# Performance work log

Measured on AMD Instinct MI355X. Metric: run time of the kernel, lower is better.

## Reference

```python
import jax, jax.numpy as jnp
import numpy as np
import math

B, L, IN_DIM, OUT_DIM = 2, 2048, 128, 128
H, DH = 8, 32            # num_heads, dim_head
ED = H * DH * 2          # embed_dim = 512
DEPTH = 1
LAMBDA_INIT = 0.8 - 0.6 * math.exp(-0.3 * (DEPTH + 1))
EPS = 1e-8


def setup_inputs() -> dict:
    key = jax.random.key(0)
    ks = jax.random.split(key, 10)
    x = jax.random.normal(ks[0], (B, 1, L, IN_DIM), dtype=jnp.float32)
    mask_2d = jax.random.bernoulli(ks[1], 0.9, (B, L, L))
    Wq = jax.random.normal(ks[2], (IN_DIM, ED), dtype=jnp.float32) * 0.05
    Wkv = jax.random.normal(ks[3], (IN_DIM, 2 * ED), dtype=jnp.float32) * 0.05
    Wout = jax.random.normal(ks[4], (ED, OUT_DIM), dtype=jnp.float32) * 0.05
    lambda_q1 = jax.random.normal(ks[5], (DH,), dtype=jnp.float32) * 0.1
    lambda_k1 = jax.random.normal(ks[6], (DH,), dtype=jnp.float32) * 0.1
    lambda_q2 = jax.random.normal(ks[7], (DH,), dtype=jnp.float32) * 0.1
    lambda_k2 = jax.random.normal(ks[8], (DH,), dtype=jnp.float32) * 0.1
    gamma = jnp.ones((2 * DH,), dtype=jnp.float32)
    return {"x": x, "mask_2d": mask_2d, "Wq": Wq, "Wkv": Wkv, "Wout": Wout,
            "lambda_q1": lambda_q1, "lambda_k1": lambda_k1,
            "lambda_q2": lambda_q2, "lambda_k2": lambda_k2, "gamma": gamma}


def reference(x, mask_2d, Wq, Wkv, Wout, lambda_q1, lambda_k1, lambda_q2, lambda_k2, gamma):
    b = x.shape[0]
    xs = x[:, 0]                                   # [b, L, in_dim]
    q = xs @ Wq                                    # [b, L, 2*H*DH]
    k, v = jnp.split(xs @ Wkv, 2, axis=-1)
    q = q.reshape(b, L, 2 * H, DH).transpose(0, 2, 1, 3) * (DH ** -0.5)  # [b,2H,L,d]
    k = k.reshape(b, L, 2 * H, DH).transpose(0, 2, 1, 3)                 # [b,2H,L,d]
    v = v.reshape(b, L, H, 2 * DH).transpose(0, 2, 1, 3)                 # [b,H,L,2d]
    dots = jnp.einsum('bnld,bnmd->bnlm', q, k)     # [b,2H,L,L]
    mask_value = -jnp.finfo(dots.dtype).max
    dots = jnp.where(mask_2d[:, None, :, :], dots, mask_value)
    attn_w = jax.nn.softmax(dots.astype(jnp.float32), axis=-1).astype(dots.dtype)
    lam1 = jnp.exp(jnp.sum(lambda_q1 * lambda_k1))
    lam2 = jnp.exp(jnp.sum(lambda_q2 * lambda_k2))
    lam = lam1 - lam2 + LAMBDA_INIT
    attn_w = attn_w.reshape(b, H, 2, L, L)
    attn_w = attn_w[:, :, 0] - lam * attn_w[:, :, 1]   # [b,H,L,L]
    attn = jnp.einsum('bhlm,bhmd->bhld', attn_w, v)    # [b,H,L,2d]
    rms = jnp.sqrt(jnp.mean(attn ** 2, axis=-1, keepdims=True))
    attn = gamma * (attn / (rms + EPS)) * (1.0 - LAMBDA_INIT)
    out = attn.transpose(0, 2, 1, 3).reshape(b, L, H * 2 * DH) @ Wout  # [b,L,out_dim]
    return out[:, None]                             # [b,1,L,out_dim]
```

## Files before the change

kernel.cpp:

```cpp
#include <hip/hip_runtime.h>
#include <float.h>
#include <math.h>

typedef __attribute__((ext_vector_type(8))) short short8;
typedef __attribute__((ext_vector_type(4))) float f32x4;

constexpr int SEQL = 2048;
constexpr int NQH  = 16;
constexpr int NVH  = 8;
constexpr int DHD  = 32;
constexpr float LAMB_INIT = 0.4707130183436648f;
constexpr float REPS      = 1e-8f;
constexpr float QW        = 0.25503492f;

static __device__ __forceinline__ unsigned short f2bf(float f) {
    union { float f; unsigned u; } a; a.f = f;
    unsigned u = a.u;
    u += 0x7fffu + ((u >> 16) & 1u);
    return (unsigned short)(u >> 16);
}

static __device__ __forceinline__ unsigned cvtpk(float lo, float hi) {
    unsigned r;
    asm("v_cvt_pk_bf16_f32 %0, %1, %2" : "=v"(r) : "v"(lo), "v"(hi));
    return r;
}

static __device__ __forceinline__ float expv(float x) {
    float r;
    asm("v_exp_f32 %0, %1" : "=v"(r) : "v"(x));
    return r;
}

static __device__ __forceinline__ void stage16(const unsigned short* g, unsigned short* l) {
    __builtin_amdgcn_global_load_lds(
        (const __attribute__((address_space(1))) unsigned int*)g,
        (__attribute__((address_space(3))) unsigned int*)l, 16, 0, 0);
}

__global__ __launch_bounds__(256) void wprep_kernel(
        const float* __restrict__ Wq, const float* __restrict__ Wkv,
        const float* __restrict__ Wout,
        unsigned short* __restrict__ Wf, unsigned short* __restrict__ WfO) {
    int gtid = blockIdx.x * 256 + threadIdx.x;
    if (gtid < 49152) {
        int kq = gtid / 1536, cc = gtid - kq * 1536;
        int k0 = kq * 4;
        float v[4];
        #pragma unroll
        for (int i = 0; i < 4; ++i)
            v[i] = (cc < 512) ? Wq[(size_t)(k0 + i) * 512 + cc] * QW
                              : Wkv[(size_t)(k0 + i) * 1024 + (cc - 512)];
        int cp = cc >> 4, lr = cc & 15, kk = k0 >> 5, lg = (k0 >> 3) & 3, j0 = k0 & 7;
        uint2 pk;
        pk.x = cvtpk(v[0], v[1]); pk.y = cvtpk(v[2], v[3]);
        *(uint2*)(Wf + (((size_t)(cp * 4 + kk) * 4 + lg) * 16 + lr) * 8 + j0) = pk;
    }
    if (gtid < 16384) {
        int cc = gtid & 127, k0 = (gtid >> 7) * 4;
        float v[4];
        #pragma unroll
        for (int i = 0; i < 4; ++i) v[i] = Wout[(size_t)(k0 + i) * 128 + cc];
        int cp = cc >> 4, lr = cc & 15, kk = k0 >> 5, lg = (k0 >> 3) & 3, j0 = k0 & 7;
        uint2 pk;
        pk.x = cvtpk(v[0], v[1]); pk.y = cvtpk(v[2], v[3]);
        *(uint2*)(WfO + (((size_t)(cp * 16 + kk) * 4 + lg) * 16 + lr) * 8 + j0) = pk;
    }
}

__global__ __launch_bounds__(256) void qkv_mask_kernel(
        const float* __restrict__ x, const unsigned short* __restrict__ Wf,
        const unsigned char* __restrict__ mb, const int* __restrict__ mi,
        unsigned long long* __restrict__ bits,
        unsigned short* __restrict__ Q, unsigned short* __restrict__ Kf,
        unsigned short* __restrict__ Vf) {
    __shared__ int cnt[256];
    int t = threadIdx.x, w = t >> 6, lane = t & 63, lr = lane & 15, lg = lane >> 4;
    {
        int c = 0;
        #pragma unroll
        for (int i = 0; i < 16; ++i) c += (mb[t * 16 + i] != 0);
        cnt[t] = c;
    }
    __syncthreads();
    for (int s = 128; s > 0; s >>= 1) { if (t < s) cnt[t] += cnt[t + s]; __syncthreads(); }
    int f = cnt[0] > 2048;
    int lid = blockIdx.x;
    int swz = (lid & 7) * 192 + (lid >> 3);
    int by = swz >> 6, bx = swz & 63;
    int r0 = bx * 64 + w * 16;
    short8 ax[4];
    #pragma unroll
    for (int kk = 0; kk < 4; ++kk) {
        const float* xp = x + (size_t)(r0 + lr) * 128 + kk * 32 + lg * 8;
        float4 v0 = *(const float4*)xp;
        float4 v1 = *(const float4*)(xp + 4);
        union { short8 v; unsigned u[4]; } ua;
        ua.u[0] = cvtpk(v0.x, v0.y);
        ua.u[1] = cvtpk(v0.z, v0.w);
        ua.u[2] = cvtpk(v1.x, v1.y);
        ua.u[3] = cvtpk(v1.z, v1.w);
        ax[kk] = ua.v;
    }
    f32x4 acc[4];
    #pragma unroll
    for (int ct = 0; ct < 4; ++ct) acc[ct] = (f32x4){0.f, 0.f, 0.f, 0.f};
    if (by < 16) {
        #pragma unroll
        for (int ct = 0; ct < 4; ++ct)
            #pragma unroll
            for (int kk = 0; kk < 4; ++kk) {
                short8 bw = *(const short8*)(Wf + (size_t)((by * 4 + ct) * 4 + kk) * 512 + lane * 8);
                acc[ct] = __builtin_amdgcn_mfma_f32_16x16x32_bf16(bw, ax[kk], acc[ct], 0, 0, 0);
            }
        int l = (r0 + lr) & 2047;
        int b = (r0 + lr) >> 11;
        if (by < 8) {
            #pragma unroll
            for (int ct = 0; ct < 4; ++ct) {
                int col = by * 64 + ct * 16 + 4 * lg;
                int n = col >> 5, d = col & 31;
                uint2 pk;
                pk.x = cvtpk(acc[ct][0], acc[ct][1]);
                pk.y = cvtpk(acc[ct][2], acc[ct][3]);
                *(uint2*)(Q + (((size_t)(b * NQH + n)) * SEQL + l) * DHD + d) = pk;
            }
        } else {
            size_t lpart = (size_t)((l >> 6) * 4 + ((l >> 4) & 3)) * 512 + (l & 15) * 8;
            #pragma unroll
            for (int ct = 0; ct < 4; ++ct) {
                int ck = by * 64 + ct * 16 + 4 * lg - 512;
                int n = ck >> 5, dk = ck & 31;
                uint2 pk;
                pk.x = cvtpk(acc[ct][0], acc[ct][1]);
                pk.y = cvtpk(acc[ct][2], acc[ct][3]);
                *(uint2*)(Kf + ((size_t)(b * NQH + n)) * 65536 + lpart
                             + (dk >> 3) * 128 + (dk & 7)) = pk;
            }
        }
    } else {
        #pragma unroll
        for (int ct = 0; ct < 4; ++ct)
            #pragma unroll
            for (int kk = 0; kk < 4; ++kk) {
                short8 bw = *(const short8*)(Wf + (size_t)((by * 4 + ct) * 4 + kk) * 512 + lane * 8);
                acc[ct] = __builtin_amdgcn_mfma_f32_16x16x32_bf16(ax[kk], bw, acc[ct], 0, 0, 0);
            }
        int gr0 = r0 + 4 * lg;
        int b = gr0 >> 11, l0 = gr0 & 2047;
        size_t lpart = (size_t)((l0 >> 6) * 2 + ((l0 >> 5) & 1)) * 2048
                     + ((l0 >> 4) & 1) * 4 + ((l0 >> 2) & 3) * 128;
        #pragma unroll
        for (int ct = 0; ct < 4; ++ct) {
            int cv = by * 64 + 16 * ct + lr - 1024;
            int h = cv >> 6, d = cv & 63;
            uint2 pk;
            pk.x = cvtpk(acc[ct][0], acc[ct][1]);
            pk.y = cvtpk(acc[ct][2], acc[ct][3]);
            *(uint2*)(Vf + ((size_t)(b * NVH + h)) * 131072
                         + (size_t)(d >> 4) * 512 + (d & 15) * 8 + lpart) = pk;
        }
    }
    int wd0 = blockIdx.x * 4 + w;
    for (int wd = wd0; wd < 131072; wd += 6144) {
        int e = wd * 64 + lane;
        int v = f ? (int)mb[e] : mi[e];
        unsigned long long bl = __ballot(v != 0);
        if (lane == 0) bits[wd] = bl;
    }
}

__global__ __launch_bounds__(256, 2) void attn_kernel(
        const unsigned short* __restrict__ Q, const unsigned short* __restrict__ Kf,
        const unsigned short* __restrict__ Vf, const unsigned long long* __restrict__ bits,
        const float* __restrict__ lq1, const float* __restrict__ lk1,
        const float* __restrict__ lq2, const float* __restrict__ lk2,
        const float* __restrict__ gamma, unsigned short* __restrict__ A) {
    __shared__ unsigned short lds[4][8192];
    int tid = threadIdx.x;
    int w = tid >> 6, lane = tid & 63;
    int lr = lane & 15, lg = lane >> 4;
    int lid = blockIdx.y * 32 + blockIdx.x;
    int swz = (lid & 7) * 64 + (lid >> 3);
    int qtile = swz & 31, bh = swz >> 5;
    int b = bh >> 3, h = bh & 7;
    int q0 = qtile * 64 + w * 16;
    int bnA = b * NQH + 2 * h;

    short8 aqA = *(const short8*)(Q + (((size_t)bnA) * SEQL + q0 + lr) * DHD + lg * 8);
    short8 aqB = *(const short8*)(Q + (((size_t)(bnA + 1)) * SEQL + q0 + lr) * DHD + lg * 8);
    const unsigned short* KA = Kf + ((size_t)bnA) * 65536;
    const unsigned short* KB = KA + 65536;
    const unsigned short* VB = Vf + ((size_t)(b * NVH + h)) * 131072;
    const unsigned long long* mrow = bits + ((size_t)b * SEQL + q0 + lr) * 32;

    short8 one8;
    #pragma unroll
    for (int i = 0; i < 8; ++i) one8[i] = (short)0x3F80;

    auto stage_tile = [&](int bf, int it) {
        #pragma unroll
        for (int j = 0; j < 4; ++j) {
            int c = 4 * w + j;
            const unsigned short* src =
                (c < 4) ? (KA + (size_t)it * 2048 + c * 512)
              : (c < 8) ? (KB + (size_t)it * 2048 + (c - 4) * 512)
                        : (VB + (size_t)it * 4096 + (c - 8) * 512);
            stage16(src + lane * 8, &lds[bf][c * 512]);
        }
    };

    f32x4 oA[4], oB[4], sumA, sumB;
    #pragma unroll
    for (int m = 0; m < 4; ++m) { oA[m] = (f32x4){0,0,0,0}; oB[m] = (f32x4){0,0,0,0}; }
    sumA = (f32x4){0,0,0,0}; sumB = (f32x4){0,0,0,0};
    unsigned long long mw = mrow[0];

    short8 paE[4], paO[4], bvE[8], bvO[8];
    #pragma unroll
    for (int i = 0; i < 4; ++i) { paE[i] = (short8){0,0,0,0,0,0,0,0}; paO[i] = (short8){0,0,0,0,0,0,0,0}; }
    #pragma unroll
    for (int i = 0; i < 8; ++i) { bvE[i] = (short8){0,0,0,0,0,0,0,0}; bvO[i] = (short8){0,0,0,0,0,0,0,0}; }

    stage_tile(0, 0);
    stage_tile(1, 1);

    auto body = [&](int t, short8* pa, short8* pbv, short8* npa, short8* nbv) {
        unsigned long long mwc = mw;
        mw = mrow[(t + 1) & 31];
        stage_tile((t + 2) & 3, (t + 2) & 31);
        asm volatile("s_waitcnt vmcnt(10)" ::: "memory");
        __builtin_amdgcn_s_barrier();
        __builtin_amdgcn_sched_barrier(0);
        const unsigned short* L = &lds[t & 3][0];
        short8 bkA[4], bkB[4];
        #pragma unroll
        for (int c = 0; c < 4; ++c) bkA[c] = *(const short8*)(L + c * 512 + lane * 8);
        #pragma unroll
        for (int c = 0; c < 4; ++c) bkB[c] = *(const short8*)(L + 2048 + c * 512 + lane * 8);
        #pragma unroll
        for (int z = 0; z < 8; ++z) nbv[z] = *(const short8*)(L + 4096 + z * 512 + lane * 8);
        f32x4 sA[4], sB[4];
        __builtin_amdgcn_s_setprio(1);
        #pragma unroll
        for (int c = 0; c < 4; ++c)
            sA[c] = __builtin_amdgcn_mfma_f32_16x16x32_bf16(bkA[c], aqA, (f32x4){0,0,0,0}, 0, 0, 0);
        #pragma unroll
        for (int c = 0; c < 4; ++c)
            sB[c] = __builtin_amdgcn_mfma_f32_16x16x32_bf16(bkB[c], aqB, (f32x4){0,0,0,0}, 0, 0, 0);
        #pragma unroll
        for (int m = 0; m < 4; ++m) {
            oA[m] = __builtin_amdgcn_mfma_f32_16x16x32_bf16(pa[0], pbv[m], oA[m], 0, 0, 0);
            oB[m] = __builtin_amdgcn_mfma_f32_16x16x32_bf16(pa[2], pbv[m], oB[m], 0, 0, 0);
        }
        #pragma unroll
        for (int m = 0; m < 4; ++m) {
            oA[m] = __builtin_amdgcn_mfma_f32_16x16x32_bf16(pa[1], pbv[4 + m], oA[m], 0, 0, 0);
            oB[m] = __builtin_amdgcn_mfma_f32_16x16x32_bf16(pa[3], pbv[4 + m], oB[m], 0, 0, 0);
        }
        __builtin_amdgcn_s_setprio(0);
        unsigned long long mwl = mwc >> (4 * lg);
        unsigned mlo = (unsigned)mwl, mhi = (unsigned)(mwl >> 32);
        float pA[4][4], pB[4][4];
        #pragma unroll
        for (int c = 0; c < 4; ++c) {
            unsigned wv = (c < 2) ? mlo : mhi;
            int sh = (c & 1) * 16;
            #pragma unroll
            for (int r = 0; r < 4; ++r) {
                unsigned keep = (wv >> (sh + r)) & 1u;
                float eA = expv(sA[c][r]);
                float eB = expv(sB[c][r]);
                pA[c][r] = keep ? eA : 0.f;
                pB[c][r] = keep ? eB : 0.f;
            }
        }
        union { short8 v; unsigned u[4]; } a0, a1, b0, b1;
        a0.u[0] = cvtpk(pA[0][0], pA[0][1]); a0.u[1] = cvtpk(pA[0][2], pA[0][3]);
        a0.u[2] = cvtpk(pA[1][0], pA[1][1]); a0.u[3] = cvtpk(pA[1][2], pA[1][3]);
        a1.u[0] = cvtpk(pA[2][0], pA[2][1]); a1.u[1] = cvtpk(pA[2][2], pA[2][3]);
        a1.u[2] = cvtpk(pA[3][0], pA[3][1]); a1.u[3] = cvtpk(pA[3][2], pA[3][3]);
        b0.u[0] = cvtpk(pB[0][0], pB[0][1]); b0.u[1] = cvtpk(pB[0][2], pB[0][3]);
        b0.u[2] = cvtpk(pB[1][0], pB[1][1]); b0.u[3] = cvtpk(pB[1][2], pB[1][3]);
        b1.u[0] = cvtpk(pB[2][0], pB[2][1]); b1.u[1] = cvtpk(pB[2][2], pB[2][3]);
        b1.u[2] = cvtpk(pB[3][0], pB[3][1]); b1.u[3] = cvtpk(pB[3][2], pB[3][3]);
        sumA = __builtin_amdgcn_mfma_f32_16x16x32_bf16(a0.v, one8, sumA, 0, 0, 0);
        sumA = __builtin_amdgcn_mfma_f32_16x16x32_bf16(a1.v, one8, sumA, 0, 0, 0);
        sumB = __builtin_amdgcn_mfma_f32_16x16x32_bf16(b0.v, one8, sumB, 0, 0, 0);
        sumB = __builtin_amdgcn_mfma_f32_16x16x32_bf16(b1.v, one8, sumB, 0, 0, 0);
        npa[0] = a0.v; npa[1] = a1.v; npa[2] = b0.v; npa[3] = b1.v;
    };

    for (int tp = 0; tp < 16; ++tp) {
        body(2 * tp,     paE, bvE, paO, bvO);
        body(2 * tp + 1, paO, bvO, paE, bvE);
    }
    #pragma unroll
    for (int m = 0; m < 4; ++m) {
        oA[m] = __builtin_amdgcn_mfma_f32_16x16x32_bf16(paE[0], bvE[m], oA[m], 0, 0, 0);
        oB[m] = __builtin_amdgcn_mfma_f32_16x16x32_bf16(paE[2], bvE[m], oB[m], 0, 0, 0);
    }
    #pragma unroll
    for (int m = 0; m < 4; ++m) {
        oA[m] = __builtin_amdgcn_mfma_f32_16x16x32_bf16(paE[1], bvE[4 + m], oA[m], 0, 0, 0);
        oB[m] = __builtin_amdgcn_mfma_f32_16x16x32_bf16(paE[3], bvE[4 + m], oB[m], 0, 0, 0);
    }
    asm volatile("s_waitcnt vmcnt(0)" ::: "memory");
    float iA[4], iB[4];
    #pragma unroll
    for (int r = 0; r < 4; ++r) {
        iA[r] = 1.f / sumA[r];
        iB[r] = 1.f / sumB[r];
    }
    int l31 = lane & 31;
    float t1 = lq1[l31] * lk1[l31];
    float t2 = lq2[l31] * lk2[l31];
    #pragma unroll
    for (int o = 1; o < 32; o <<= 1) { t1 += __shfl_xor(t1, o, 64); t2 += __shfl_xor(t2, o, 64); }
    float lam = __expf(t1) - __expf(t2) + LAMB_INIT;
    float dv[4][4];
    float sq[4] = {0.f, 0.f, 0.f, 0.f};
    #pragma unroll
    for (int m = 0; m < 4; ++m)
        #pragma unroll
        for (int r = 0; r < 4; ++r) {
            float v = oA[m][r] * iA[r] - lam * (oB[m][r] * iB[r]);
            dv[m][r] = v;
            sq[r] += v * v;
        }
    #pragma unroll
    for (int r = 0; r < 4; ++r) {
        #pragma unroll
        for (int o = 1; o < 16; o <<= 1) sq[r] += __shfl_xor(sq[r], o, 64);
        sq[r] = (1.f - LAMB_INIT) / (sqrtf(sq[r] * (1.f / 64.f)) + REPS);
    }
    float gm[4];
    #pragma unroll
    for (int m = 0; m < 4; ++m) gm[m] = gamma[16 * m + lr];
    unsigned short* Ab = A + ((size_t)(b * SEQL + q0 + 4 * lg)) * 512 + h * 64 + lr;
    #pragma unroll
    for (int m = 0; m < 4; ++m)
        #pragma unroll
        for (int r = 0; r < 4; ++r)
            Ab[(size_t)r * 512 + 16 * m] = f2bf(dv[m][r] * sq[r] * gm[m]);
}

__global__ __launch_bounds__(256) void proj_mfma_kernel(
        const unsigned short* __restrict__ Ab, const unsigned short* __restrict__ WfO,
        float* __restrict__ out) {
    __shared__ f32x4 red[1536];
    int t = threadIdx.x, w = t >> 6, lane = t & 63, lr = lane & 15, lg = lane >> 4;
    int r0 = blockIdx.x * 16;
    f32x4 acc[8];
    #pragma unroll
    for (int ct = 0; ct < 8; ++ct) acc[ct] = (f32x4){0.f, 0.f, 0.f, 0.f};
    #pragma unroll
    for (int j = 0; j < 4; ++j) {
        int kk = w * 4 + j;
        short8 af = *(const short8*)(Ab + (size_t)(r0 + lr) * 512 + kk * 32 + lg * 8);
        #pragma unroll
        for (int ct = 0; ct < 8; ++ct) {
            short8 bf = *(const short8*)(WfO + (size_t)(ct * 16 + kk) * 512 + lane * 8);
            acc[ct] = __builtin_amdgcn_mfma_f32_16x16x32_bf16(bf, af, acc[ct], 0, 0, 0);
        }
    }
    if (w) {
        #pragma unroll
        for (int ct = 0; ct < 8; ++ct)
            red[((w - 1) * 8 + ct) * 64 + lane] = acc[ct];
    }
    __syncthreads();
    if (w) return;
    #pragma unroll
    for (int ct = 0; ct < 8; ++ct) {
        #pragma unroll
        for (int j = 0; j < 3; ++j) {
            f32x4 pv = red[(j * 8 + ct) * 64 + lane];
            acc[ct][0] += pv[0]; acc[ct][1] += pv[1];
            acc[ct][2] += pv[2]; acc[ct][3] += pv[3];
        }
        float4 st = { acc[ct][0], acc[ct][1], acc[ct][2], acc[ct][3] };
        *(float4*)(out + (size_t)(r0 + lr) * 128 + ct * 16 + 4 * lg) = st;
    }
}

extern "C" void kernel_launch(void* const* d_in, const int* in_sizes, int n_in,
                              void* d_out, int out_size, void* d_ws, size_t ws_size,
                              hipStream_t stream) {
    const float* x    = (const float*)d_in[0];
    const void*  mask = d_in[1];
    const float* Wq   = (const float*)d_in[2];
    const float* Wkv  = (const float*)d_in[3];
    const float* Wout = (const float*)d_in[4];
    const float* lq1  = (const float*)d_in[5];
    const float* lk1  = (const float*)d_in[6];
    const float* lq2  = (const float*)d_in[7];
    const float* lk2  = (const float*)d_in[8];
    const float* gam  = (const float*)d_in[9];
    float* out = (float*)d_out;

    char* wsb = (char*)d_ws;
    unsigned long long* bits = (unsigned long long*)(wsb + 4096);
    unsigned short* Q        = (unsigned short*)(wsb + 1052672);
    unsigned short* Kf       = (unsigned short*)(wsb + 5246976);
    unsigned short* Vf       = (unsigned short*)(wsb + 9441280);
    unsigned short* Wf       = (unsigned short*)(wsb + 14684160);
    unsigned short* WfO      = (unsigned short*)(wsb + 15077376);
    unsigned short* Ab       = (unsigned short*)(wsb + 15208448);

    wprep_kernel<<<256, 256, 0, stream>>>(Wq, Wkv, Wout, Wf, WfO);
    qkv_mask_kernel<<<1536, 256, 0, stream>>>(x, Wf,
                                              (const unsigned char*)mask,
                                              (const int*)mask, bits, Q, Kf, Vf);
    attn_kernel<<<dim3(32, 16), 256, 0, stream>>>(Q, Kf, Vf, bits,
                                                  lq1, lk1, lq2, lk2, gam, Ab);
    proj_mfma_kernel<<<256, 256, 0, stream>>>(Ab, WfO, out);
}
```

Baseline: 86.88 us.

## Fuse weight prep into QKV kernel and split projection over output tiles

Removes the separate weight-prep launch. Each QKV block now converts its own 64-column slice of Wq/Wkv to bf16 in LDS, and the Wout conversion moves to the tail of the QKV kernel. The projection kernel no longer does a K-split with an LDS reduction: each wave computes one 16x16 output tile over the full K, using twice as many blocks. This saves one launch and the reduction sync, at the cost of every QKV block redundantly converting its weight slice, which adds global reads of fp32 weights.

```diff
diff --git a/kernel.cpp b/kernel.cpp
--- a/kernel.cpp
+++ b/kernel.cpp
@@ -38,42 +38,14 @@
         (__attribute__((address_space(3))) unsigned int*)l, 16, 0, 0);
 }
 
-__global__ __launch_bounds__(256) void wprep_kernel(
-        const float* __restrict__ Wq, const float* __restrict__ Wkv,
-        const float* __restrict__ Wout,
-        unsigned short* __restrict__ Wf, unsigned short* __restrict__ WfO) {
-    int gtid = blockIdx.x * 256 + threadIdx.x;
-    if (gtid < 49152) {
-        int kq = gtid / 1536, cc = gtid - kq * 1536;
-        int k0 = kq * 4;
-        float v[4];
-        #pragma unroll
-        for (int i = 0; i < 4; ++i)
-            v[i] = (cc < 512) ? Wq[(size_t)(k0 + i) * 512 + cc] * QW
-                              : Wkv[(size_t)(k0 + i) * 1024 + (cc - 512)];
-        int cp = cc >> 4, lr = cc & 15, kk = k0 >> 5, lg = (k0 >> 3) & 3, j0 = k0 & 7;
-        uint2 pk;
-        pk.x = cvtpk(v[0], v[1]); pk.y = cvtpk(v[2], v[3]);
-        *(uint2*)(Wf + (((size_t)(cp * 4 + kk) * 4 + lg) * 16 + lr) * 8 + j0) = pk;
-    }
-    if (gtid < 16384) {
-        int cc = gtid & 127, k0 = (gtid >> 7) * 4;
-        float v[4];
-        #pragma unroll
-        for (int i = 0; i < 4; ++i) v[i] = Wout[(size_t)(k0 + i) * 128 + cc];
-        int cp = cc >> 4, lr = cc & 15, kk = k0 >> 5, lg = (k0 >> 3) & 3, j0 = k0 & 7;
-        uint2 pk;
-        pk.x = cvtpk(v[0], v[1]); pk.y = cvtpk(v[2], v[3]);
-        *(uint2*)(WfO + (((size_t)(cp * 16 + kk) * 4 + lg) * 16 + lr) * 8 + j0) = pk;
-    }
-}
-
 __global__ __launch_bounds__(256) void qkv_mask_kernel(
-        const float* __restrict__ x, const unsigned short* __restrict__ Wf,
+        const float* __restrict__ x, const float* __restrict__ Wq,
+        const float* __restrict__ Wkv, const float* __restrict__ Wout,
         const unsigned char* __restrict__ mb, const int* __restrict__ mi,
         unsigned long long* __restrict__ bits,
         unsigned short* __restrict__ Q, unsigned short* __restrict__ Kf,
-        unsigned short* __restrict__ Vf) {
+        unsigned short* __restrict__ Vf, unsigned short* __restrict__ WfO) {
+    __shared__ unsigned short wlds[8192];
     __shared__ int cnt[256];
     int t = threadIdx.x, w = t >> 6, lane = t & 63, lr = lane & 15, lg = lane >> 4;
     {
@@ -88,6 +60,27 @@
     int lid = blockIdx.x;
     int swz = (lid & 7) * 192 + (lid >> 3);
     int by = swz >> 6, bx = swz & 63;
+    {
+        const float* wsrc; int wstride, c0; float wscale;
+        if (by < 8)       { wsrc = Wq;  wstride = 512;  c0 = by * 64;          wscale = QW;  }
+        else if (by < 16) { wsrc = Wkv; wstride = 1024; c0 = (by - 8) * 64;    wscale = 1.f; }
+        else              { wsrc = Wkv; wstride = 1024; c0 = 512 + (by - 16) * 64; wscale = 1.f; }
+        #pragma unroll
+        for (int i = 0; i < 8; ++i) {
+            int q = t + i * 256;
+            int kq = q >> 6, c = q & 63;
+            int k0 = kq * 4;
+            const float* p = wsrc + (size_t)k0 * wstride + c0 + c;
+            float v0 = p[0] * wscale;
+            float v1 = p[wstride] * wscale;
+            float v2 = p[2 * wstride] * wscale;
+            float v3 = p[3 * wstride] * wscale;
+            int ct = c >> 4, clr = c & 15, kk = k0 >> 5, klg = (k0 >> 3) & 3, j0 = k0 & 7;
+            uint2 pk;
+            pk.x = cvtpk(v0, v1); pk.y = cvtpk(v2, v3);
+            *(uint2*)(wlds + (size_t)(ct * 4 + kk) * 512 + klg * 128 + clr * 8 + j0) = pk;
+        }
+    }
     int r0 = bx * 64 + w * 16;
     short8 ax[4];
     #pragma unroll
@@ -102,6 +95,7 @@
         ua.u[3] = cvtpk(v1.z, v1.w);
         ax[kk] = ua.v;
     }
+    __syncthreads();
     f32x4 acc[4];
     #pragma unroll
     for (int ct = 0; ct < 4; ++ct) acc[ct] = (f32x4){0.f, 0.f, 0.f, 0.f};
@@ -110,7 +104,7 @@
         for (int ct = 0; ct < 4; ++ct)
             #pragma unroll
             for (int kk = 0; kk < 4; ++kk) {
-                short8 bw = *(const short8*)(Wf + (size_t)((by * 4 + ct) * 4 + kk) * 512 + lane * 8);
+                short8 bw = *(const short8*)(wlds + (size_t)(ct * 4 + kk) * 512 + lane * 8);
                 acc[ct] = __builtin_amdgcn_mfma_f32_16x16x32_bf16(bw, ax[kk], acc[ct], 0, 0, 0);
             }
         int l = (r0 + lr) & 2047;
@@ -143,7 +137,7 @@
         for (int ct = 0; ct < 4; ++ct)
             #pragma unroll
             for (int kk = 0; kk < 4; ++kk) {
-                short8 bw = *(const short8*)(Wf + (size_t)((by * 4 + ct) * 4 + kk) * 512 + lane * 8);
+                short8 bw = *(const short8*)(wlds + (size_t)(ct * 4 + kk) * 512 + lane * 8);
                 acc[ct] = __builtin_amdgcn_mfma_f32_16x16x32_bf16(ax[kk], bw, acc[ct], 0, 0, 0);
             }
         int gr0 = r0 + 4 * lg;
@@ -167,6 +161,18 @@
         int v = f ? (int)mb[e] : mi[e];
         unsigned long long bl = __ballot(v != 0);
         if (lane == 0) bits[wd] = bl;
+    }
+    int g2 = blockIdx.x * 256 + t;
+    if (g2 < 16384) {
+        int cc = g2 & 127, k0 = (g2 >> 7) * 4;
+        float v0 = Wout[(size_t)k0 * 128 + cc];
+        float v1 = Wout[(size_t)(k0 + 1) * 128 + cc];
+        float v2 = Wout[(size_t)(k0 + 2) * 128 + cc];
+        float v3 = Wout[(size_t)(k0 + 3) * 128 + cc];
+        int cp = cc >> 4, clr = cc & 15, kk = k0 >> 5, klg = (k0 >> 3) & 3, j0 = k0 & 7;
+        uint2 pk;
+        pk.x = cvtpk(v0, v1); pk.y = cvtpk(v2, v3);
+        *(uint2*)(WfO + (size_t)(cp * 16 + kk) * 512 + klg * 128 + clr * 8 + j0) = pk;
     }
 }
 
@@ -348,40 +354,19 @@
 __global__ __launch_bounds__(256) void proj_mfma_kernel(
         const unsigned short* __restrict__ Ab, const unsigned short* __restrict__ WfO,
         float* __restrict__ out) {
-    __shared__ f32x4 red[1536];
     int t = threadIdx.x, w = t >> 6, lane = t & 63, lr = lane & 15, lg = lane >> 4;
-    int r0 = blockIdx.x * 16;
-    f32x4 acc[8];
-    #pragma unroll
-    for (int ct = 0; ct < 8; ++ct) acc[ct] = (f32x4){0.f, 0.f, 0.f, 0.f};
-    #pragma unroll
-    for (int j = 0; j < 4; ++j) {
-        int kk = w * 4 + j;
+    int bid = blockIdx.x;
+    int r0 = (bid >> 1) * 16;
+    int ct = (bid & 1) * 4 + w;
+    f32x4 acc = (f32x4){0.f, 0.f, 0.f, 0.f};
+    #pragma unroll
+    for (int kk = 0; kk < 16; ++kk) {
         short8 af = *(const short8*)(Ab + (size_t)(r0 + lr) * 512 + kk * 32 + lg * 8);
-        #pragma unroll
-        for (int ct = 0; ct < 8; ++ct) {
-            short8 bf = *(const short8*)(WfO + (size_t)(ct * 16 + kk) * 512 + lane * 8);
-            acc[ct] = __builtin_amdgcn_mfma_f32_16x16x32_bf16(bf, af, acc[ct], 0, 0, 0);
-        }
-    }
-    if (w) {
-        #pragma unroll
-        for (int ct = 0; ct < 8; ++ct)
-            red[((w - 1) * 8 + ct) * 64 + lane] = acc[ct];
-    }
-    __syncthreads();
-    if (w) return;
-    #pragma unroll
-    for (int ct = 0; ct < 8; ++ct) {
-        #pragma unroll
-        for (int j = 0; j < 3; ++j) {
-            f32x4 pv = red[(j * 8 + ct) * 64 + lane];
-            acc[ct][0] += pv[0]; acc[ct][1] += pv[1];
-            acc[ct][2] += pv[2]; acc[ct][3] += pv[3];
-        }
-        float4 st = { acc[ct][0], acc[ct][1], acc[ct][2], acc[ct][3] };
-        *(float4*)(out + (size_t)(r0 + lr) * 128 + ct * 16 + 4 * lg) = st;
-    }
+        short8 bf = *(const short8*)(WfO + (size_t)(ct * 16 + kk) * 512 + lane * 8);
+        acc = __builtin_amdgcn_mfma_f32_16x16x32_bf16(bf, af, acc, 0, 0, 0);
+    }
+    float4 st = { acc[0], acc[1], acc[2], acc[3] };
+    *(float4*)(out + (size_t)(r0 + lr) * 128 + ct * 16 + 4 * lg) = st;
 }
 
 extern "C" void kernel_launch(void* const* d_in, const int* in_sizes, int n_in,
@@ -404,15 +389,13 @@
     unsigned short* Q        = (unsigned short*)(wsb + 1052672);
     unsigned short* Kf       = (unsigned short*)(wsb + 5246976);
     unsigned short* Vf       = (unsigned short*)(wsb + 9441280);
-    unsigned short* Wf       = (unsigned short*)(wsb + 14684160);
     unsigned short* WfO      = (unsigned short*)(wsb + 15077376);
     unsigned short* Ab       = (unsigned short*)(wsb + 15208448);
 
-    wprep_kernel<<<256, 256, 0, stream>>>(Wq, Wkv, Wout, Wf, WfO);
-    qkv_mask_kernel<<<1536, 256, 0, stream>>>(x, Wf,
+    qkv_mask_kernel<<<1536, 256, 0, stream>>>(x, Wq, Wkv, Wout,
                                               (const unsigned char*)mask,
-                                              (const int*)mask, bits, Q, Kf, Vf);
+                                              (const int*)mask, bits, Q, Kf, Vf, WfO);
     attn_kernel<<<dim3(32, 16), 256, 0, stream>>>(Q, Kf, Vf, bits,
                                                   lq1, lk1, lq2, lk2, gam, Ab);
-    proj_mfma_kernel<<<256, 256, 0, stream>>>(Ab, WfO, out);
-}
+    proj_mfma_kernel<<<512, 256, 0, stream>>>(Ab, WfO, out);
+}
```

Result: faster. 82.57 us (-5.0%).
